# Kernel tuning notes

Measured on AMD Instinct MI355X. Metric: run time of the kernel, lower is better.

The kernel has to match this reference:

```python
import jax, jax.numpy as jnp
import numpy as np

DECAY = 0.99
EPS = 1e-05


def setup_inputs() -> dict:
    key = jax.random.key(0)
    k1, k2, k3 = jax.random.split(key, 3)
    D, K = 64, 512
    input = jax.random.normal(k1, (64, 32, 32, D), dtype=jnp.float32)
    embed = jax.random.normal(k2, (D, K), dtype=jnp.float32)
    cluster_size = jnp.zeros((K,), dtype=jnp.float32)
    embed_avg = jax.random.normal(k3, (D, K), dtype=jnp.float32)
    return {"input": input, "embed": embed, "cluster_size": cluster_size, "embed_avg": embed_avg}


def reference(input, embed, cluster_size, embed_avg):
    D, K = embed.shape
    flat = input.reshape(-1, D)  # [N, D]
    dist = (
        jnp.sum(flat * flat, axis=1, keepdims=True)
        - 2.0 * (flat @ embed)
        + jnp.sum(embed * embed, axis=0, keepdims=True)
    )
    embed_ind = jnp.argmin(dist, axis=1)  # [N]
    quantize = jnp.take(embed.T, embed_ind, axis=0).reshape(input.shape)
    embed_ind_out = embed_ind.reshape(input.shape[:-1])

    # training-mode EMA codebook update (equivalent to one-hot matmuls, done as scatter)
    onehot_sum = jax.ops.segment_sum(jnp.ones_like(embed_ind, dtype=flat.dtype), embed_ind, num_segments=K)  # [K]
    embed_sum = jax.ops.segment_sum(flat, embed_ind, num_segments=K).T  # [D, K]
    new_cluster_size = cluster_size * DECAY + (1.0 - DECAY) * onehot_sum
    new_embed_avg = embed_avg * DECAY + (1.0 - DECAY) * embed_sum
    n = jnp.sum(new_cluster_size)
    cs = (new_cluster_size + EPS) / (n + K * EPS) * n
    embed_new = new_embed_avg / cs[None, :]

    diff = jnp.mean((jax.lax.stop_gradient(quantize) - input) ** 2)
    quantize_st = input + jax.lax.stop_gradient(quantize - input)
    return quantize_st, diff, embed_ind_out, embed_new, new_cluster_size, new_embed_avg
```

## Files before the change

kernel.cpp:

```cpp
#include <hip/hip_runtime.h>
#include <hip/hip_bf16.h>

#define KC 512

#define OFF_Q     0
#define OFF_DIFF  4194304
#define OFF_IND   4194305
#define OFF_ENEW  4259841
#define OFF_NCS   4292609
#define OFF_NAVG  4293121

#define WS_ET    0
#define WS_C     32768
#define WS_CNT   33280
#define WS_ESUM  33792
#define WS_DIFF  66560
#define WS_NTOT  66561
#define WS_EB    66576

typedef __attribute__((ext_vector_type(8))) short bf16x8;
typedef __attribute__((ext_vector_type(4))) float f32x4;

union U4B { uint4 u; bf16x8 b; };

__device__ __forceinline__ unsigned short f2bf(float x) {
    __hip_bfloat16 h = __float2bfloat16(x);
    union { __hip_bfloat16 h; unsigned short s; } cv; cv.h = h; return cv.s;
}
__device__ __forceinline__ float bf2f(unsigned short s) {
    union { unsigned int u; float f; } cv; cv.u = ((unsigned int)s) << 16; return cv.f;
}

__global__ __launch_bounds__(256) void k_prep(const float* __restrict__ embed,
                                              float* __restrict__ ws) {
    int i = blockIdx.x * 256 + threadIdx.x;
    if (i < 512 + 32768 + 2) ws[WS_CNT + i] = 0.0f;
    if (i < 32768) {
        int k = i >> 6, d = i & 63;
        ws[WS_ET + i] = embed[d * KC + k];
    }
    if (i < 512) {
        float s = 0.0f;
        #pragma unroll
        for (int d = 0; d < 64; ++d) { float e = embed[d * KC + i]; s = fmaf(e, e, s); }
        ws[WS_C + i] = 0.5f * s;
    }
    if (i < 8192) {
        int term = i >> 12;
        int r = i & 4095;
        int ct = r >> 7, ks = (r >> 6) & 1, ln = r & 63;
        int col = ct * 16 + (ln & 15);
        int d0 = ks * 32 + ((ln >> 4) & 3) * 8;
        unsigned int w[4];
        #pragma unroll
        for (int p = 0; p < 4; ++p) {
            float x0 = embed[(d0 + 2 * p) * KC + col];
            float x1 = embed[(d0 + 2 * p + 1) * KC + col];
            unsigned short h0 = f2bf(x0), h1 = f2bf(x1);
            unsigned short o0, o1;
            if (term == 0) { o0 = h0; o1 = h1; }
            else { o0 = f2bf(x0 - bf2f(h0)); o1 = f2bf(x1 - bf2f(h1)); }
            w[p] = (unsigned int)o0 | ((unsigned int)o1 << 16);
        }
        uint4 u; u.x = w[0]; u.y = w[1]; u.z = w[2]; u.w = w[3];
        reinterpret_cast<uint4*>(ws + WS_EB)[i] = u;
    }
}

__global__ __launch_bounds__(512, 2) void k_main(const float* __restrict__ input,
                                                 const float* __restrict__ embed,
                                                 const uint4* __restrict__ EB,
                                                 const float* __restrict__ c,
                                                 const float* __restrict__ Et,
                                                 float* __restrict__ out,
                                                 float* __restrict__ diffsum) {
    __shared__ uint4 EBl[8192];
    __shared__ float biasl[512];
    __shared__ float sb1[8][32];
    __shared__ int   sk1[8][32];
    __shared__ float sb2[8][32];
    __shared__ float sxs[8][32];

    const int t    = threadIdx.x;
    const int lane = t & 63;
    const int wave = __builtin_amdgcn_readfirstlane(t >> 6);
    const int l15  = lane & 15;
    const int g4   = (lane >> 4) & 3;

    #pragma unroll
    for (int it = 0; it < 16; ++it) EBl[t + it * 512] = EB[t + it * 512];
    if (t < 512) biasl[t] = c[t];
    __syncthreads();

    const int R0 = blockIdx.x * 256 + wave * 32;

    bf16x8 Ah[2][2], Al[2][2];
    float px[2] = {0.0f, 0.0f};
    #pragma unroll
    for (int rt = 0; rt < 2; ++rt) {
        #pragma unroll
        for (int ks = 0; ks < 2; ++ks) {
            const float* xp = input + (size_t)(R0 + rt * 16 + l15) * 64 + ks * 32 + g4 * 8;
            float4 a = *reinterpret_cast<const float4*>(xp);
            float4 b = *reinterpret_cast<const float4*>(xp + 4);
            float vv[8] = {a.x, a.y, a.z, a.w, b.x, b.y, b.z, b.w};
            #pragma unroll
            for (int j = 0; j < 8; ++j) {
                unsigned short hi = f2bf(vv[j]);
                Ah[rt][ks][j] = (short)hi;
                Al[rt][ks][j] = (short)f2bf(vv[j] - bf2f(hi));
                px[rt] += vv[j] * vv[j];
            }
        }
    }
    px[0] += __shfl_xor(px[0], 16); px[0] += __shfl_xor(px[0], 32);
    px[1] += __shfl_xor(px[1], 16); px[1] += __shfl_xor(px[1], 32);
    if (lane < 16) { sxs[wave][lane] = px[0]; sxs[wave][16 + lane] = px[1]; }

    float B1[8], B2[8]; int K1[8];
    #pragma unroll
    for (int q = 0; q < 8; ++q) { B1[q] = -3.0e38f; B2[q] = -3.0e38f; K1[q] = 0; }

    for (int h = 0; h < 2; ++h) {
        f32x4 acc[2][16];
        #pragma unroll
        for (int ct = 0; ct < 16; ++ct) {
            float bb = biasl[(h * 16 + ct) * 16 + l15];
            f32x4 iv = {-bb, -bb, -bb, -bb};
            acc[0][ct] = iv; acc[1][ct] = iv;
        }
        #pragma unroll
        for (int ct = 0; ct < 16; ++ct) {
            #pragma unroll
            for (int ks = 0; ks < 2; ++ks) {
                int base = ((h * 16 + ct) * 2 + ks) * 64 + lane;
                U4B uh, ul;
                uh.u = EBl[base];
                ul.u = EBl[4096 + base];
                #pragma unroll
                for (int rt = 0; rt < 2; ++rt)
                    acc[rt][ct] = __builtin_amdgcn_mfma_f32_16x16x32_bf16(Ah[rt][ks], uh.b, acc[rt][ct], 0, 0, 0);
                #pragma unroll
                for (int rt = 0; rt < 2; ++rt)
                    acc[rt][ct] = __builtin_amdgcn_mfma_f32_16x16x32_bf16(Ah[rt][ks], ul.b, acc[rt][ct], 0, 0, 0);
                #pragma unroll
                for (int rt = 0; rt < 2; ++rt)
                    acc[rt][ct] = __builtin_amdgcn_mfma_f32_16x16x32_bf16(Al[rt][ks], uh.b, acc[rt][ct], 0, 0, 0);
            }
        }
        #pragma unroll
        for (int rt = 0; rt < 2; ++rt) {
            #pragma unroll
            for (int reg = 0; reg < 4; ++reg) {
                int q = rt * 4 + reg;
                #pragma unroll
                for (int ct = 0; ct < 16; ++ct) {
                    float s = acc[rt][ct][reg];
                    int k = (h * 16 + ct) * 16 + l15;
                    if (s > B1[q]) { B2[q] = B1[q]; B1[q] = s; K1[q] = k; }
                    else if (s > B2[q]) B2[q] = s;
                }
            }
        }
    }
    #pragma unroll
    for (int off = 1; off < 16; off <<= 1) {
        #pragma unroll
        for (int q = 0; q < 8; ++q) {
            float vv = __shfl_xor(B1[q], off);
            int   kk = __shfl_xor(K1[q], off);
            float v2 = __shfl_xor(B2[q], off);
            if (vv > B1[q] || (vv == B1[q] && kk < K1[q])) {
                B2[q] = fmaxf(B1[q], v2); B1[q] = vv; K1[q] = kk;
            } else {
                B2[q] = fmaxf(B2[q], vv);
            }
        }
    }
    if (l15 == 0) {
        #pragma unroll
        for (int rt = 0; rt < 2; ++rt)
            #pragma unroll
            for (int reg = 0; reg < 4; ++reg) {
                int row = rt * 16 + g4 * 4 + reg, q = rt * 4 + reg;
                sb1[wave][row] = B1[q]; sk1[wave][row] = K1[q]; sb2[wave][row] = B2[q];
            }
    }

    float dsum = 0.0f;
    for (int r = 0; r < 32; ++r) {
        const int row = R0 + r;
        float b1 = sb1[wave][r], b2 = sb2[wave][r], xs = sxs[wave][r];
        int   k1 = sk1[wave][r];
        if (b1 - b2 < 6.0e-3f) {
            float xv = input[(size_t)row * 64 + lane];
            float s[8];
            #pragma unroll
            for (int j = 0; j < 8; ++j) s[j] = -biasl[lane + 64 * j];
            for (int d = 0; d < 64; ++d) {
                float xd = __shfl(xv, d);
                #pragma unroll
                for (int j = 0; j < 8; ++j)
                    s[j] = fmaf(xd, embed[d * KC + lane + 64 * j], s[j]);
            }
            float bb = s[0]; int bk = lane;
            #pragma unroll
            for (int j = 1; j < 8; ++j) {
                int cc = lane + 64 * j;
                if (s[j] > bb) { bb = s[j]; bk = cc; }
            }
            #pragma unroll
            for (int off = 1; off < 64; off <<= 1) {
                float vv = __shfl_xor(bb, off);
                int   kk = __shfl_xor(bk, off);
                if (vv > bb || (vv == bb && kk < bk)) { bb = vv; bk = kk; }
            }
            k1 = bk; b1 = bb;
        }
        float e = Et[(size_t)k1 * 64 + lane];
        out[OFF_Q + (size_t)row * 64 + lane] = e;
        if (lane == 0) {
            out[OFF_IND + row] = (float)k1;
            dsum += xs - 2.0f * b1;
        }
    }
    if (lane == 0) atomicAdd(diffsum, dsum);
}

__global__ __launch_bounds__(256) void k_esum(const float* __restrict__ ind,
                                              const float* __restrict__ input,
                                              float* __restrict__ esum,
                                              float* __restrict__ counts) {
    __shared__ float sacc[4][64];
    __shared__ int   scnt[4];

    const int k    = blockIdx.x & 511;
    const int sl   = blockIdx.x >> 9;
    const int lane = threadIdx.x & 63;
    const int wv   = threadIdx.x >> 6;
    const float fk = (float)k;

    float accd = 0.0f;
    int cnt = 0;
    const int rbase = sl * 4096 + wv * 1024;
    #pragma unroll 4
    for (int base = rbase; base < rbase + 1024; base += 64) {
        float bkf = ind[base + lane];
        unsigned long long m = __ballot(bkf == fk);
        cnt += __popcll(m);
        while (m) {
            int b = __ffsll((unsigned long long)m) - 1;
            m &= (m - 1);
            accd += input[(size_t)(base + b) * 64 + lane];
        }
    }
    sacc[wv][lane] = accd;
    if (lane == 0) scnt[wv] = cnt;
    __syncthreads();
    if (wv == 0) {
        float s = sacc[0][lane] + sacc[1][lane] + sacc[2][lane] + sacc[3][lane];
        atomicAdd(&esum[k * 64 + lane], s);
        if (lane == 0) atomicAdd(&counts[k], (float)(scnt[0] + scnt[1] + scnt[2] + scnt[3]));
    }
}

__global__ __launch_bounds__(512) void k_ncs(const float* __restrict__ cluster_size,
                                             const float* __restrict__ ws,
                                             float* __restrict__ out,
                                             float* __restrict__ wsw) {
    __shared__ float red[512];
    int t = threadIdx.x;
    float ncs = cluster_size[t] * 0.99f + (1.0f - 0.99f) * ws[WS_CNT + t];
    out[OFF_NCS + t] = ncs;
    red[t] = ncs;
    __syncthreads();
    for (int off = 256; off > 0; off >>= 1) {
        if (t < off) red[t] += red[t + off];
        __syncthreads();
    }
    if (t == 0) {
        wsw[WS_NTOT] = red[0];
        out[OFF_DIFF] = ws[WS_DIFF] * (1.0f / 4194304.0f);
    }
}

__global__ __launch_bounds__(512) void k_emb(const float* __restrict__ embed_avg,
                                             const float* __restrict__ ws,
                                             float* __restrict__ out) {
    int d = blockIdx.x;
    int t = threadIdx.x;
    float ncs = out[OFF_NCS + t];
    float ntot = ws[WS_NTOT];
    float csk = (ncs + 1e-5f) / (ntot + 512.0f * 1e-5f) * ntot;
    int idx = d * KC + t;
    float avg = embed_avg[idx] * 0.99f + (1.0f - 0.99f) * ws[WS_ESUM + t * 64 + d];
    out[OFF_NAVG + idx] = avg;
    out[OFF_ENEW + idx] = avg / csk;
}

extern "C" void kernel_launch(void* const* d_in, const int* in_sizes, int n_in,
                              void* d_out, int out_size, void* d_ws, size_t ws_size,
                              hipStream_t stream) {
    const float* input        = (const float*)d_in[0];
    const float* embed        = (const float*)d_in[1];
    const float* cluster_size = (const float*)d_in[2];
    const float* embed_avg    = (const float*)d_in[3];
    float* out = (float*)d_out;
    float* ws  = (float*)d_ws;

    k_prep<<<131, 256, 0, stream>>>(embed, ws);
    k_main<<<256, 512, 0, stream>>>(input, embed,
                                    reinterpret_cast<const uint4*>(ws + WS_EB),
                                    ws + WS_C, ws + WS_ET, out, ws + WS_DIFF);
    k_esum<<<8192, 256, 0, stream>>>(out + OFF_IND, input, ws + WS_ESUM, ws + WS_CNT);
    k_ncs<<<1, 512, 0, stream>>>(cluster_size, ws, out, ws);
    k_emb<<<64, 512, 0, stream>>>(embed_avg, ws, out);
}
```

Measured before the change: 119.2 us.

## Stream codebook fragments from global/L2 instead of LDS, smaller blocks

The main distance kernel no longer stages the 128 KB bf16 hi/lo codebook in shared memory; each wave reads the codebook fragments directly from global memory, relying on L2/L1 caching. Blocks shrink from 512 to 256 threads, each wave handling 16 rows instead of 32, and the grid grows from 256 to 1024 blocks. This removes the per-block LDS fill and the LDS occupancy limit and cuts accumulator registers. In exchange each MFMA now waits on global loads, and codebook reuse per load drops by half.

New measurement: 239.5 us. 2.01x slower.

```diff
diff --git a/kernel.cpp b/kernel.cpp
--- a/kernel.cpp
+++ b/kernel.cpp
@@ -67,19 +67,18 @@
     }
 }
 
-__global__ __launch_bounds__(512, 2) void k_main(const float* __restrict__ input,
-                                                 const float* __restrict__ embed,
-                                                 const uint4* __restrict__ EB,
-                                                 const float* __restrict__ c,
-                                                 const float* __restrict__ Et,
-                                                 float* __restrict__ out,
-                                                 float* __restrict__ diffsum) {
-    __shared__ uint4 EBl[8192];
+__global__ __launch_bounds__(256) void k_main(const float* __restrict__ input,
+                                              const float* __restrict__ embed,
+                                              const uint4* __restrict__ EB,
+                                              const float* __restrict__ c,
+                                              const float* __restrict__ Et,
+                                              float* __restrict__ out,
+                                              float* __restrict__ diffsum) {
     __shared__ float biasl[512];
-    __shared__ float sb1[8][32];
-    __shared__ int   sk1[8][32];
-    __shared__ float sb2[8][32];
-    __shared__ float sxs[8][32];
+    __shared__ float sb1[4][16];
+    __shared__ int   sk1[4][16];
+    __shared__ float sb2[4][16];
+    __shared__ float sxs[4][16];
 
     const int t    = threadIdx.x;
     const int lane = t & 63;
@@ -87,86 +86,72 @@
     const int l15  = lane & 15;
     const int g4   = (lane >> 4) & 3;
 
+    biasl[t] = c[t];
+    biasl[t + 256] = c[t + 256];
+    __syncthreads();
+
+    const int R0 = blockIdx.x * 64 + wave * 16;
+
+    bf16x8 Ah[2], Al[2];
+    float px = 0.0f;
     #pragma unroll
-    for (int it = 0; it < 16; ++it) EBl[t + it * 512] = EB[t + it * 512];
-    if (t < 512) biasl[t] = c[t];
-    __syncthreads();
-
-    const int R0 = blockIdx.x * 256 + wave * 32;
-
-    bf16x8 Ah[2][2], Al[2][2];
-    float px[2] = {0.0f, 0.0f};
+    for (int ks = 0; ks < 2; ++ks) {
+        const float* xp = input + (size_t)(R0 + l15) * 64 + ks * 32 + g4 * 8;
+        float4 a = *reinterpret_cast<const float4*>(xp);
+        float4 b = *reinterpret_cast<const float4*>(xp + 4);
+        float vv[8] = {a.x, a.y, a.z, a.w, b.x, b.y, b.z, b.w};
+        #pragma unroll
+        for (int j = 0; j < 8; ++j) {
+            unsigned short hi = f2bf(vv[j]);
+            Ah[ks][j] = (short)hi;
+            Al[ks][j] = (short)f2bf(vv[j] - bf2f(hi));
+            px += vv[j] * vv[j];
+        }
+    }
+    px += __shfl_xor(px, 16); px += __shfl_xor(px, 32);
+    if (lane < 16) sxs[wave][lane] = px;
+
+    float B1[4], B2[4]; int K1[4];
     #pragma unroll
-    for (int rt = 0; rt < 2; ++rt) {
-        #pragma unroll
-        for (int ks = 0; ks < 2; ++ks) {
-            const float* xp = input + (size_t)(R0 + rt * 16 + l15) * 64 + ks * 32 + g4 * 8;
-            float4 a = *reinterpret_cast<const float4*>(xp);
-            float4 b = *reinterpret_cast<const float4*>(xp + 4);
-            float vv[8] = {a.x, a.y, a.z, a.w, b.x, b.y, b.z, b.w};
-            #pragma unroll
-            for (int j = 0; j < 8; ++j) {
-                unsigned short hi = f2bf(vv[j]);
-                Ah[rt][ks][j] = (short)hi;
-                Al[rt][ks][j] = (short)f2bf(vv[j] - bf2f(hi));
-                px[rt] += vv[j] * vv[j];
-            }
-        }
-    }
-    px[0] += __shfl_xor(px[0], 16); px[0] += __shfl_xor(px[0], 32);
-    px[1] += __shfl_xor(px[1], 16); px[1] += __shfl_xor(px[1], 32);
-    if (lane < 16) { sxs[wave][lane] = px[0]; sxs[wave][16 + lane] = px[1]; }
-
-    float B1[8], B2[8]; int K1[8];
-    #pragma unroll
-    for (int q = 0; q < 8; ++q) { B1[q] = -3.0e38f; B2[q] = -3.0e38f; K1[q] = 0; }
-
+    for (int q = 0; q < 4; ++q) { B1[q] = -3.0e38f; B2[q] = -3.0e38f; K1[q] = 0; }
+
+    #pragma unroll 1
     for (int h = 0; h < 2; ++h) {
-        f32x4 acc[2][16];
+        f32x4 acc[16];
         #pragma unroll
         for (int ct = 0; ct < 16; ++ct) {
             float bb = biasl[(h * 16 + ct) * 16 + l15];
             f32x4 iv = {-bb, -bb, -bb, -bb};
-            acc[0][ct] = iv; acc[1][ct] = iv;
-        }
-        #pragma unroll
+            acc[ct] = iv;
+        }
+        #pragma unroll 2
         for (int ct = 0; ct < 16; ++ct) {
             #pragma unroll
             for (int ks = 0; ks < 2; ++ks) {
                 int base = ((h * 16 + ct) * 2 + ks) * 64 + lane;
                 U4B uh, ul;
-                uh.u = EBl[base];
-                ul.u = EBl[4096 + base];
-                #pragma unroll
-                for (int rt = 0; rt < 2; ++rt)
-                    acc[rt][ct] = __builtin_amdgcn_mfma_f32_16x16x32_bf16(Ah[rt][ks], uh.b, acc[rt][ct], 0, 0, 0);
-                #pragma unroll
-                for (int rt = 0; rt < 2; ++rt)
-                    acc[rt][ct] = __builtin_amdgcn_mfma_f32_16x16x32_bf16(Ah[rt][ks], ul.b, acc[rt][ct], 0, 0, 0);
-                #pragma unroll
-                for (int rt = 0; rt < 2; ++rt)
-                    acc[rt][ct] = __builtin_amdgcn_mfma_f32_16x16x32_bf16(Al[rt][ks], uh.b, acc[rt][ct], 0, 0, 0);
-            }
-        }
-        #pragma unroll
-        for (int rt = 0; rt < 2; ++rt) {
-            #pragma unroll
-            for (int reg = 0; reg < 4; ++reg) {
-                int q = rt * 4 + reg;
-                #pragma unroll
-                for (int ct = 0; ct < 16; ++ct) {
-                    float s = acc[rt][ct][reg];
-                    int k = (h * 16 + ct) * 16 + l15;
-                    if (s > B1[q]) { B2[q] = B1[q]; B1[q] = s; K1[q] = k; }
-                    else if (s > B2[q]) B2[q] = s;
-                }
+                uh.u = EB[base];
+                ul.u = EB[4096 + base];
+                acc[ct] = __builtin_amdgcn_mfma_f32_16x16x32_bf16(Ah[ks], uh.b, acc[ct], 0, 0, 0);
+                acc[ct] = __builtin_amdgcn_mfma_f32_16x16x32_bf16(Ah[ks], ul.b, acc[ct], 0, 0, 0);
+                acc[ct] = __builtin_amdgcn_mfma_f32_16x16x32_bf16(Al[ks], uh.b, acc[ct], 0, 0, 0);
+            }
+        }
+        #pragma unroll
+        for (int reg = 0; reg < 4; ++reg) {
+            #pragma unroll
+            for (int ct = 0; ct < 16; ++ct) {
+                float s = acc[ct][reg];
+                int k = (h * 16 + ct) * 16 + l15;
+                if (s > B1[reg]) { B2[reg] = B1[reg]; B1[reg] = s; K1[reg] = k; }
+                else if (s > B2[reg]) B2[reg] = s;
             }
         }
     }
     #pragma unroll
     for (int off = 1; off < 16; off <<= 1) {
         #pragma unroll
-        for (int q = 0; q < 8; ++q) {
+        for (int q = 0; q < 4; ++q) {
             float vv = __shfl_xor(B1[q], off);
             int   kk = __shfl_xor(K1[q], off);
             float v2 = __shfl_xor(B2[q], off);
@@ -179,16 +164,14 @@
     }
     if (l15 == 0) {
         #pragma unroll
-        for (int rt = 0; rt < 2; ++rt)
-            #pragma unroll
-            for (int reg = 0; reg < 4; ++reg) {
-                int row = rt * 16 + g4 * 4 + reg, q = rt * 4 + reg;
-                sb1[wave][row] = B1[q]; sk1[wave][row] = K1[q]; sb2[wave][row] = B2[q];
-            }
+        for (int reg = 0; reg < 4; ++reg) {
+            int row = g4 * 4 + reg;
+            sb1[wave][row] = B1[reg]; sk1[wave][row] = K1[reg]; sb2[wave][row] = B2[reg];
+        }
     }
 
     float dsum = 0.0f;
-    for (int r = 0; r < 32; ++r) {
+    for (int r = 0; r < 16; ++r) {
         const int row = R0 + r;
         float b1 = sb1[wave][r], b2 = sb2[wave][r], xs = sxs[wave][r];
         int   k1 = sk1[wave][r];
@@ -309,9 +292,9 @@
     float* ws  = (float*)d_ws;
 
     k_prep<<<131, 256, 0, stream>>>(embed, ws);
-    k_main<<<256, 512, 0, stream>>>(input, embed,
-                                    reinterpret_cast<const uint4*>(ws + WS_EB),
-                                    ws + WS_C, ws + WS_ET, out, ws + WS_DIFF);
+    k_main<<<1024, 256, 0, stream>>>(input, embed,
+                                     reinterpret_cast<const uint4*>(ws + WS_EB),
+                                     ws + WS_C, ws + WS_ET, out, ws + WS_DIFF);
     k_esum<<<8192, 256, 0, stream>>>(out + OFF_IND, input, ws + WS_ESUM, ws + WS_CNT);
     k_ncs<<<1, 512, 0, stream>>>(cluster_size, ws, out, ws);
     k_emb<<<64, 512, 0, stream>>>(embed_avg, ws, out);
```
